# Kernel optimization log

Hardware: AMD Instinct MI355X
Metric: run time of the kernel (lower is better)

Reference implementation:

```python
import jax, jax.numpy as jnp
import numpy as np

B, V, DEMB, H, LAT, L = 16384, 64, 128, 512, 128, 2
PAD, BOS, EOS = 0, 1, 2


def setup_inputs() -> dict:
    key = jax.random.key(0)
    ks = jax.random.split(key, 12)
    s = 0.05  # small init so softmax logits stay well-scaled
    z = jax.random.normal(ks[0], (B, LAT), jnp.float32)
    E = jax.random.normal(ks[1], (V, DEMB), jnp.float32) * s
    E = E.at[PAD].set(0.0)  # padding_idx row is zero
    W_l2h = jax.random.normal(ks[2], (H, LAT), jnp.float32) * s
    b_l2h = jnp.zeros((H,), jnp.float32)
    W_ih0 = jax.random.normal(ks[3], (4 * H, DEMB), jnp.float32) * s
    W_hh0 = jax.random.normal(ks[4], (4 * H, H), jnp.float32) * s
    b_ih0 = jnp.zeros((4 * H,), jnp.float32)
    b_hh0 = jnp.zeros((4 * H,), jnp.float32)
    W_ih1 = jax.random.normal(ks[5], (4 * H, H), jnp.float32) * s
    W_hh1 = jax.random.normal(ks[6], (4 * H, H), jnp.float32) * s
    b_ih1 = jnp.zeros((4 * H,), jnp.float32)
    b_hh1 = jnp.zeros((4 * H,), jnp.float32)
    W_out = jax.random.normal(ks[7], (V, H), jnp.float32) * s
    b_out = jnp.zeros((V,), jnp.float32)
    return {"z": z, "E": E, "W_l2h": W_l2h, "b_l2h": b_l2h,
            "W_ih0": W_ih0, "W_hh0": W_hh0, "b_ih0": b_ih0, "b_hh0": b_hh0,
            "W_ih1": W_ih1, "W_hh1": W_hh1, "b_ih1": b_ih1, "b_hh1": b_hh1,
            "W_out": W_out, "b_out": b_out, "max_len": 100}


def _lstm_cell(x, h, c, Wih, Whh, bih, bhh):
    # torch LSTM gate order: i, f, g, o
    g = x @ Wih.T + bih + h @ Whh.T + bhh  # [B, 4H]
    i, f, gg, o = jnp.split(g, 4, axis=-1)
    c_new = jax.nn.sigmoid(f) * c + jax.nn.sigmoid(i) * jnp.tanh(gg)
    h_new = jax.nn.sigmoid(o) * jnp.tanh(c_new)
    return h_new, c_new


def reference(z, E, W_l2h, b_l2h, W_ih0, W_hh0, b_ih0, b_hh0,
              W_ih1, W_hh1, b_ih1, b_hh1, W_out, b_out, max_len):
    # initial states: c0 = latent2hidden(z) repeated over layers, h0 = 0
    c0 = z @ W_l2h.T + b_l2h                      # [B, H]
    c = jnp.stack([c0, c0])                       # [L, B, H]
    h = jnp.zeros_like(c)
    prev = jnp.full((B,), BOS, jnp.int32)
    is_end = jnp.zeros((B,), bool)
    keys = jax.random.split(jax.random.key(42), max_len)

    def step(carry, k):
        h, c, prev, is_end = carry
        x = E[prev]                               # [B, DEMB]
        h0, c0_ = _lstm_cell(x, h[0], c[0], W_ih0, W_hh0, b_ih0, b_hh0)
        h1, c1_ = _lstm_cell(h0, h[1], c[1], W_ih1, W_hh1, b_ih1, b_hh1)
        logits = h1 @ W_out.T + b_out             # [B, V]
        cur = jax.random.categorical(k, logits)   # same dist as Categorical(softmax(logits))
        is_end = is_end | (cur == EOS)            # mark eos; eos itself becomes pad
        cur = jnp.where(is_end, PAD, cur).astype(jnp.int32)
        return (jnp.stack([h0, h1]), jnp.stack([c0_, c1_]), cur, is_end), cur

    _, samples = jax.lax.scan(step, (h, c, prev, is_end), keys)  # [T, B]
    return samples.T                              # [B, T]
```

## Files before the change

kernel.cpp:

```cpp
#include <hip/hip_runtime.h>
#include <stdint.h>

#define B_    16384
#define V_    64
#define DEMB_ 128
#define H_    512
#define PAD_  0
#define BOS_  1
#define EOS_  2

__device__ __forceinline__ uint32_t rotl32(uint32_t v, int n) {
    return (v << n) | (v >> (32 - n));
}

__device__ __forceinline__ void tf2x32(uint32_t k0, uint32_t k1,
                                       uint32_t x0, uint32_t x1,
                                       uint32_t& o0, uint32_t& o1)
{
    const uint32_t k2 = k0 ^ k1 ^ 0x1BD11BDAu;
    x0 += k0; x1 += k1;
#define TFR(r) { x0 += x1; x1 = rotl32(x1, (r)); x1 ^= x0; }
    TFR(13) TFR(15) TFR(26) TFR(6)
    x0 += k1; x1 += k2 + 1u;
    TFR(17) TFR(29) TFR(16) TFR(24)
    x0 += k2; x1 += k0 + 2u;
    TFR(13) TFR(15) TFR(26) TFR(6)
    x0 += k0; x1 += k1 + 3u;
    TFR(17) TFR(29) TFR(16) TFR(24)
    x0 += k1; x1 += k2 + 4u;
    TFR(13) TFR(15) TFR(26) TFR(6)
    x0 += k2; x1 += k0 + 5u;
#undef TFR
    o0 = x0; o1 = x1;
}

__device__ __forceinline__ float sigm(float x) {
    return 1.0f / (1.0f + expf(-x));
}

__global__ __launch_bounds__(256)
void init_state(const float* __restrict__ z, const float* __restrict__ Wl,
                const float* __restrict__ bl,
                float* __restrict__ C0, float* __restrict__ C1,
                float* __restrict__ H0, float* __restrict__ H1)
{
    __shared__ __align__(16) float As[16][68];
    __shared__ __align__(16) float Bs[16][68];
    const int tid  = threadIdx.x;
    const int b0   = blockIdx.x * 64;
    const int j0   = blockIdx.y * 64;
    const int tx   = tid & 15, ty = tid >> 4;
    const int lrow = tid >> 2, lkq = tid & 3;

    float acc[4][4] = {};

    for (int kt = 0; kt < DEMB_ / 16; ++kt) {
        const int k0 = kt * 16;
        float4 av = *reinterpret_cast<const float4*>(z  + (size_t)(b0 + lrow) * DEMB_ + k0 + lkq * 4);
        float4 bv = *reinterpret_cast<const float4*>(Wl + (size_t)(j0 + lrow) * DEMB_ + k0 + lkq * 4);
        __syncthreads();
        As[lkq*4+0][lrow] = av.x; As[lkq*4+1][lrow] = av.y; As[lkq*4+2][lrow] = av.z; As[lkq*4+3][lrow] = av.w;
        Bs[lkq*4+0][lrow] = bv.x; Bs[lkq*4+1][lrow] = bv.y; Bs[lkq*4+2][lrow] = bv.z; Bs[lkq*4+3][lrow] = bv.w;
        __syncthreads();
#pragma unroll
        for (int kk = 0; kk < 16; ++kk) {
            float4 a4 = *reinterpret_cast<const float4*>(&As[kk][ty*4]);
            float4 b4 = *reinterpret_cast<const float4*>(&Bs[kk][tx*4]);
            float ar[4] = {a4.x, a4.y, a4.z, a4.w};
            float br[4] = {b4.x, b4.y, b4.z, b4.w};
#pragma unroll
            for (int r = 0; r < 4; ++r)
#pragma unroll
                for (int c = 0; c < 4; ++c)
                    acc[r][c] = fmaf(ar[r], br[c], acc[r][c]);
        }
    }

#pragma unroll
    for (int r = 0; r < 4; ++r) {
        const int b = b0 + ty * 4 + r;
        const int j = j0 + tx * 4;
        float v0 = acc[r][0] + bl[j+0];
        float v1 = acc[r][1] + bl[j+1];
        float v2 = acc[r][2] + bl[j+2];
        float v3 = acc[r][3] + bl[j+3];
        float4 cv = {v0, v1, v2, v3};
        float4 zz = {0.f, 0.f, 0.f, 0.f};
        *reinterpret_cast<float4*>(C0 + (size_t)b * H_ + j) = cv;
        *reinterpret_cast<float4*>(C1 + (size_t)b * H_ + j) = cv;
        *reinterpret_cast<float4*>(H0 + (size_t)b * H_ + j) = zz;
        *reinterpret_cast<float4*>(H1 + (size_t)b * H_ + j) = zz;
    }
}

__global__ __launch_bounds__(256)
void init_tokens(int* __restrict__ prevtok, int* __restrict__ isend)
{
    int i = blockIdx.x * 256 + threadIdx.x;
    if (i < B_) { prevtok[i] = BOS_; isend[i] = 0; }
}

template<int KX, bool GATHER>
__global__ __launch_bounds__(256, 2)
void lstm_layer(const float* __restrict__ Asrc,
                const int*   __restrict__ prevtok,
                const float* __restrict__ Hrec,
                const float* __restrict__ Wih,
                const float* __restrict__ Whh,
                const float* __restrict__ bih,
                const float* __restrict__ bhh,
                float* __restrict__ Cst,
                float* __restrict__ Hout)
{
    __shared__ __align__(16) float As[16][132];
    __shared__ __align__(16) float Bs[4][16][68];
    __shared__ int rowtok[128];

    const int tid  = threadIdx.x;
    const int b0   = blockIdx.x * 128;
    const int j0   = blockIdx.y * 64;
    const int tx   = tid & 15;
    const int ty   = tid >> 4;
    const int srow = tid >> 1;
    const int sk   = (tid & 1) * 8;

    if (GATHER) {
        if (tid < 128) rowtok[tid] = prevtok[b0 + tid];
        __syncthreads();
    }

    const int NT = (KX + H_) / 16;

    float4 av[2], bv[4];
    {
        const int k0 = 0;
        const float* arow = GATHER ? (Asrc + (size_t)rowtok[srow] * DEMB_)
                                   : (Asrc + (size_t)(b0 + srow) * KX);
        av[0] = *reinterpret_cast<const float4*>(arow + k0 + sk);
        av[1] = *reinterpret_cast<const float4*>(arow + k0 + sk + 4);
#pragma unroll
        for (int h = 0; h < 2; ++h) {
            const int grow = srow + h * 128;
            const int g = grow >> 6, u = grow & 63;
            const float* brow = Wih + (size_t)(g * H_ + j0 + u) * KX + k0 + sk;
            bv[h*2+0] = *reinterpret_cast<const float4*>(brow);
            bv[h*2+1] = *reinterpret_cast<const float4*>(brow + 4);
        }
    }

    float acc[4][8][4] = {};

    for (int kt = 0; kt < NT; ++kt) {
        __syncthreads();
        {
            float a0[4] = {av[0].x, av[0].y, av[0].z, av[0].w};
            float a1[4] = {av[1].x, av[1].y, av[1].z, av[1].w};
#pragma unroll
            for (int i = 0; i < 4; ++i) {
                As[sk + i][srow]     = a0[i];
                As[sk + 4 + i][srow] = a1[i];
            }
#pragma unroll
            for (int h = 0; h < 2; ++h) {
                const int grow = srow + h * 128;
                const int g = grow >> 6, u = grow & 63;
                float b0r[4] = {bv[h*2+0].x, bv[h*2+0].y, bv[h*2+0].z, bv[h*2+0].w};
                float b1r[4] = {bv[h*2+1].x, bv[h*2+1].y, bv[h*2+1].z, bv[h*2+1].w};
#pragma unroll
                for (int i = 0; i < 4; ++i) {
                    Bs[g][sk + i][u]     = b0r[i];
                    Bs[g][sk + 4 + i][u] = b1r[i];
                }
            }
        }
        __syncthreads();

        if (kt + 1 < NT) {
            const int k0n = (kt + 1) * 16;
            if (k0n < KX) {
                const float* arow = GATHER ? (Asrc + (size_t)rowtok[srow] * DEMB_)
                                           : (Asrc + (size_t)(b0 + srow) * KX);
                av[0] = *reinterpret_cast<const float4*>(arow + k0n + sk);
                av[1] = *reinterpret_cast<const float4*>(arow + k0n + sk + 4);
#pragma unroll
                for (int h = 0; h < 2; ++h) {
                    const int grow = srow + h * 128;
                    const int g = grow >> 6, u = grow & 63;
                    const float* brow = Wih + (size_t)(g * H_ + j0 + u) * KX + k0n + sk;
                    bv[h*2+0] = *reinterpret_cast<const float4*>(brow);
                    bv[h*2+1] = *reinterpret_cast<const float4*>(brow + 4);
                }
            } else {
                const int kh = k0n - KX;
                av[0] = *reinterpret_cast<const float4*>(Hrec + (size_t)(b0 + srow) * H_ + kh + sk);
                av[1] = *reinterpret_cast<const float4*>(Hrec + (size_t)(b0 + srow) * H_ + kh + sk + 4);
#pragma unroll
                for (int h = 0; h < 2; ++h) {
                    const int grow = srow + h * 128;
                    const int g = grow >> 6, u = grow & 63;
                    const float* brow = Whh + (size_t)(g * H_ + j0 + u) * H_ + kh + sk;
                    bv[h*2+0] = *reinterpret_cast<const float4*>(brow);
                    bv[h*2+1] = *reinterpret_cast<const float4*>(brow + 4);
                }
            }
        }

#pragma unroll 4
        for (int kk = 0; kk < 16; ++kk) {
            float4 a40 = *reinterpret_cast<const float4*>(&As[kk][ty*8]);
            float4 a41 = *reinterpret_cast<const float4*>(&As[kk][ty*8+4]);
            float ar[8] = {a40.x, a40.y, a40.z, a40.w, a41.x, a41.y, a41.z, a41.w};
#pragma unroll
            for (int g = 0; g < 4; ++g) {
                float4 b4 = *reinterpret_cast<const float4*>(&Bs[g][kk][tx*4]);
                float br[4] = {b4.x, b4.y, b4.z, b4.w};
#pragma unroll
                for (int r = 0; r < 8; ++r)
#pragma unroll
                    for (int c = 0; c < 4; ++c)
                        acc[g][r][c] = fmaf(ar[r], br[c], acc[g][r][c]);
            }
        }
    }

    const int j = j0 + tx * 4;
    float4 bi0 = *reinterpret_cast<const float4*>(bih + 0*H_ + j);
    float4 bi1 = *reinterpret_cast<const float4*>(bih + 1*H_ + j);
    float4 bi2 = *reinterpret_cast<const float4*>(bih + 2*H_ + j);
    float4 bi3 = *reinterpret_cast<const float4*>(bih + 3*H_ + j);
    float4 bh0 = *reinterpret_cast<const float4*>(bhh + 0*H_ + j);
    float4 bh1 = *reinterpret_cast<const float4*>(bhh + 1*H_ + j);
    float4 bh2 = *reinterpret_cast<const float4*>(bhh + 2*H_ + j);
    float4 bh3 = *reinterpret_cast<const float4*>(bhh + 3*H_ + j);
    float bi[4][4] = {{bi0.x,bi0.y,bi0.z,bi0.w},{bi1.x,bi1.y,bi1.z,bi1.w},
                      {bi2.x,bi2.y,bi2.z,bi2.w},{bi3.x,bi3.y,bi3.z,bi3.w}};
    float bh[4][4] = {{bh0.x,bh0.y,bh0.z,bh0.w},{bh1.x,bh1.y,bh1.z,bh1.w},
                      {bh2.x,bh2.y,bh2.z,bh2.w},{bh3.x,bh3.y,bh3.z,bh3.w}};

#pragma unroll
    for (int r = 0; r < 8; ++r) {
        const int b = b0 + ty * 8 + r;
        float4 c4 = *reinterpret_cast<const float4*>(Cst + (size_t)b * H_ + j);
        float cold[4] = {c4.x, c4.y, c4.z, c4.w};
        float cn[4], hn[4];
#pragma unroll
        for (int c = 0; c < 4; ++c) {
            float gi = acc[0][r][c] + bi[0][c] + bh[0][c];
            float gf = acc[1][r][c] + bi[1][c] + bh[1][c];
            float gg = acc[2][r][c] + bi[2][c] + bh[2][c];
            float go = acc[3][r][c] + bi[3][c] + bh[3][c];
            float si = sigm(gi), sf = sigm(gf), so = sigm(go);
            float tg = tanhf(gg);
            float cc = __fadd_rn(__fmul_rn(sf, cold[c]), __fmul_rn(si, tg));
            cn[c] = cc;
            hn[c] = __fmul_rn(so, tanhf(cc));
        }
        float4 co = {cn[0], cn[1], cn[2], cn[3]};
        float4 ho = {hn[0], hn[1], hn[2], hn[3]};
        *reinterpret_cast<float4*>(Cst  + (size_t)b * H_ + j) = co;
        *reinterpret_cast<float4*>(Hout + (size_t)b * H_ + j) = ho;
    }
}

__global__ __launch_bounds__(256)
void sample_step(const float* __restrict__ H1src, const float* __restrict__ Wout,
                 const float* __restrict__ bout,
                 int* __restrict__ prevtok, int* __restrict__ isend,
                 int* __restrict__ out, int t, int T)
{
    __shared__ __align__(16) float As[16][68];
    __shared__ __align__(16) float Bs[16][68];
    __shared__ float LG[64][65];

    const int tid  = threadIdx.x;
    const int b0   = blockIdx.x * 64;
    const int tx   = tid & 15, ty = tid >> 4;
    const int lrow = tid >> 2, lkq = tid & 3;

    float acc[4][4] = {};

    for (int kt = 0; kt < H_ / 16; ++kt) {
        const int k0 = kt * 16;
        float4 av = *reinterpret_cast<const float4*>(H1src + (size_t)(b0 + lrow) * H_ + k0 + lkq * 4);
        float4 bv = *reinterpret_cast<const float4*>(Wout  + (size_t)lrow * H_ + k0 + lkq * 4);
        __syncthreads();
        As[lkq*4+0][lrow] = av.x; As[lkq*4+1][lrow] = av.y; As[lkq*4+2][lrow] = av.z; As[lkq*4+3][lrow] = av.w;
        Bs[lkq*4+0][lrow] = bv.x; Bs[lkq*4+1][lrow] = bv.y; Bs[lkq*4+2][lrow] = bv.z; Bs[lkq*4+3][lrow] = bv.w;
        __syncthreads();
#pragma unroll
        for (int kk = 0; kk < 16; ++kk) {
            float4 a4 = *reinterpret_cast<const float4*>(&As[kk][ty*4]);
            float4 b4 = *reinterpret_cast<const float4*>(&Bs[kk][tx*4]);
            float ar[4] = {a4.x, a4.y, a4.z, a4.w};
            float br[4] = {b4.x, b4.y, b4.z, b4.w};
#pragma unroll
            for (int r = 0; r < 4; ++r)
#pragma unroll
                for (int c = 0; c < 4; ++c)
                    acc[r][c] = fmaf(ar[r], br[c], acc[r][c]);
        }
    }

#pragma unroll
    for (int r = 0; r < 4; ++r)
#pragma unroll
        for (int c = 0; c < 4; ++c)
            LG[ty*4 + r][tx*4 + c] = acc[r][c] + bout[tx*4 + c];
    __syncthreads();

    const int wv = tid >> 6, lane = tid & 63;
    uint32_t kt0, kt1;
    tf2x32(0u, 42u, 0u, (uint32_t)t, kt0, kt1);

    const float TINY = 1.1754943508222875e-38f;
    for (int rr = 0; rr < 16; ++rr) {
        const int r = wv * 16 + rr;
        const int b = b0 + r;
        float lg = LG[r][lane];
        uint32_t r0, r1;
        tf2x32(kt0, kt1, 0u, (uint32_t)(b * V_ + lane), r0, r1);
        uint32_t bits = r0 ^ r1;
        float f = __uint_as_float((bits >> 9) | 0x3f800000u) - 1.0f;
        float u = fmaxf(TINY, __fadd_rn(f, TINY));
        float g = -logf(-logf(u));
        float val = __fadd_rn(g, lg);
        int idx = lane;
#pragma unroll
        for (int off = 32; off > 0; off >>= 1) {
            float ov = __shfl_xor(val, off, 64);
            int   oi = __shfl_xor(idx, off, 64);
            if (ov > val || (ov == val && oi < idx)) { val = ov; idx = oi; }
        }
        if (lane == 0) {
            int cur = idx;
            int e   = isend[b];
            int en  = e | (cur == EOS_);
            int tok = en ? PAD_ : cur;
            isend[b]   = en;
            prevtok[b] = tok;
            out[(size_t)b * T + t] = tok;
        }
    }
}

extern "C" void kernel_launch(void* const* d_in, const int* in_sizes, int n_in,
                              void* d_out, int out_size, void* d_ws, size_t ws_size,
                              hipStream_t stream)
{
    (void)in_sizes; (void)n_in; (void)ws_size;
    const float* z    = (const float*)d_in[0];
    const float* E    = (const float*)d_in[1];
    const float* Wl2h = (const float*)d_in[2];
    const float* bl2h = (const float*)d_in[3];
    const float* Wih0 = (const float*)d_in[4];
    const float* Whh0 = (const float*)d_in[5];
    const float* bih0 = (const float*)d_in[6];
    const float* bhh0 = (const float*)d_in[7];
    const float* Wih1 = (const float*)d_in[8];
    const float* Whh1 = (const float*)d_in[9];
    const float* bih1 = (const float*)d_in[10];
    const float* bhh1 = (const float*)d_in[11];
    const float* Wout = (const float*)d_in[12];
    const float* bout = (const float*)d_in[13];
    int* out = (int*)d_out;
    const int T = out_size / B_;

    char* w = (char*)d_ws;
    const size_t S = (size_t)B_ * H_ * sizeof(float);
    float* C0  = (float*)(w + 0 * S);
    float* C1  = (float*)(w + 1 * S);
    float* H0A = (float*)(w + 2 * S);
    float* H0B = (float*)(w + 3 * S);
    float* H1A = (float*)(w + 4 * S);
    float* H1B = (float*)(w + 5 * S);
    int* prevtok = (int*)(w + 6 * S);
    int* isend   = (int*)(w + 6 * S + (size_t)B_ * sizeof(int));

    dim3 blk(256);
    init_state<<<dim3(B_/64, H_/64), blk, 0, stream>>>(z, Wl2h, bl2h, C0, C1, H0A, H1A);
    init_tokens<<<dim3(B_/256), blk, 0, stream>>>(prevtok, isend);

    float *h0c = H0A, *h0n = H0B, *h1c = H1A, *h1n = H1B;
    for (int t = 0; t < T; ++t) {
        lstm_layer<DEMB_, true><<<dim3(B_/128, H_/64), blk, 0, stream>>>(
            E, prevtok, h0c, Wih0, Whh0, bih0, bhh0, C0, h0n);
        lstm_layer<H_, false><<<dim3(B_/128, H_/64), blk, 0, stream>>>(
            h0n, nullptr, h1c, Wih1, Whh1, bih1, bhh1, C1, h1n);
        sample_step<<<dim3(B_/64), blk, 0, stream>>>(
            h1n, Wout, bout, prevtok, isend, out, t, T);
        float* tmp;
        tmp = h0c; h0c = h0n; h0n = tmp;
        tmp = h1c; h1c = h1n; h1n = tmp;
    }
}
```

Baseline: 134.1 ms.

## Double-buffer LDS tiles in LSTM GEMM and reorder block indexing

The LSTM layer GEMM now keeps two LDS tile buffers and prefetches two tiles ahead, so the next tile is written to shared memory while the current one is consumed, leaving one barrier per k-step instead of two. The grid becomes 1D with the 8 hidden-column blocks of the same batch rows placed on consecutive block IDs, so the activation rows they share stay hot in cache. LDS use per block roughly doubles, which could limit occupancy under the 2-blocks launch bound. The other edits only add a load helper and do not change behaviour.

Result: no change. 132.1 ms (-1.5%).

```diff
diff --git a/kernel.cpp b/kernel.cpp
--- a/kernel.cpp
+++ b/kernel.cpp
@@ -38,6 +38,10 @@
     return 1.0f / (1.0f + expf(-x));
 }
 
+__device__ __forceinline__ float4 ld4(const float* p) {
+    return *reinterpret_cast<const float4*>(p);
+}
+
 __global__ __launch_bounds__(256)
 void init_state(const float* __restrict__ z, const float* __restrict__ Wl,
                 const float* __restrict__ bl,
@@ -56,16 +60,16 @@
 
     for (int kt = 0; kt < DEMB_ / 16; ++kt) {
         const int k0 = kt * 16;
-        float4 av = *reinterpret_cast<const float4*>(z  + (size_t)(b0 + lrow) * DEMB_ + k0 + lkq * 4);
-        float4 bv = *reinterpret_cast<const float4*>(Wl + (size_t)(j0 + lrow) * DEMB_ + k0 + lkq * 4);
+        float4 av = ld4(z  + (size_t)(b0 + lrow) * DEMB_ + k0 + lkq * 4);
+        float4 bv = ld4(Wl + (size_t)(j0 + lrow) * DEMB_ + k0 + lkq * 4);
         __syncthreads();
         As[lkq*4+0][lrow] = av.x; As[lkq*4+1][lrow] = av.y; As[lkq*4+2][lrow] = av.z; As[lkq*4+3][lrow] = av.w;
         Bs[lkq*4+0][lrow] = bv.x; Bs[lkq*4+1][lrow] = bv.y; Bs[lkq*4+2][lrow] = bv.z; Bs[lkq*4+3][lrow] = bv.w;
         __syncthreads();
 #pragma unroll
         for (int kk = 0; kk < 16; ++kk) {
-            float4 a4 = *reinterpret_cast<const float4*>(&As[kk][ty*4]);
-            float4 b4 = *reinterpret_cast<const float4*>(&Bs[kk][tx*4]);
+            float4 a4 = ld4(&As[kk][ty*4]);
+            float4 b4 = ld4(&Bs[kk][tx*4]);
             float ar[4] = {a4.x, a4.y, a4.z, a4.w};
             float br[4] = {b4.x, b4.y, b4.z, b4.w};
 #pragma unroll
@@ -80,11 +84,8 @@
     for (int r = 0; r < 4; ++r) {
         const int b = b0 + ty * 4 + r;
         const int j = j0 + tx * 4;
-        float v0 = acc[r][0] + bl[j+0];
-        float v1 = acc[r][1] + bl[j+1];
-        float v2 = acc[r][2] + bl[j+2];
-        float v3 = acc[r][3] + bl[j+3];
-        float4 cv = {v0, v1, v2, v3};
+        float4 cv = {acc[r][0] + bl[j+0], acc[r][1] + bl[j+1],
+                     acc[r][2] + bl[j+2], acc[r][3] + bl[j+3]};
         float4 zz = {0.f, 0.f, 0.f, 0.f};
         *reinterpret_cast<float4*>(C0 + (size_t)b * H_ + j) = cv;
         *reinterpret_cast<float4*>(C1 + (size_t)b * H_ + j) = cv;
@@ -112,13 +113,14 @@
                 float* __restrict__ Cst,
                 float* __restrict__ Hout)
 {
-    __shared__ __align__(16) float As[16][132];
-    __shared__ __align__(16) float Bs[4][16][68];
+    __shared__ __align__(16) float As[2][16][132];
+    __shared__ __align__(16) float Bs[2][4][16][68];
     __shared__ int rowtok[128];
 
     const int tid  = threadIdx.x;
-    const int b0   = blockIdx.x * 128;
-    const int j0   = blockIdx.y * 64;
+    const int bid  = blockIdx.x;
+    const int b0   = (bid >> 3) * 128;
+    const int j0   = (bid & 7) * 64;
     const int tx   = tid & 15;
     const int ty   = tid >> 4;
     const int srow = tid >> 1;
@@ -129,90 +131,84 @@
         __syncthreads();
     }
 
+    const int grow0 = srow, grow1 = srow + 128;
+    const int g0 = grow0 >> 6, u0 = grow0 & 63;
+    const int g1 = grow1 >> 6, u1 = grow1 & 63;
+
+    const float* arowA = GATHER ? (Asrc + (size_t)rowtok[srow] * DEMB_)
+                                : (Asrc + (size_t)(b0 + srow) * KX);
+    const float* arowH = Hrec + (size_t)(b0 + srow) * H_;
+    const float* browA0 = Wih + (size_t)(g0 * H_ + j0 + u0) * KX;
+    const float* browA1 = Wih + (size_t)(g1 * H_ + j0 + u1) * KX;
+    const float* browH0 = Whh + (size_t)(g0 * H_ + j0 + u0) * H_;
+    const float* browH1 = Whh + (size_t)(g1 * H_ + j0 + u1) * H_;
+
     const int NT = (KX + H_) / 16;
 
     float4 av[2], bv[4];
-    {
-        const int k0 = 0;
-        const float* arow = GATHER ? (Asrc + (size_t)rowtok[srow] * DEMB_)
-                                   : (Asrc + (size_t)(b0 + srow) * KX);
-        av[0] = *reinterpret_cast<const float4*>(arow + k0 + sk);
-        av[1] = *reinterpret_cast<const float4*>(arow + k0 + sk + 4);
-#pragma unroll
-        for (int h = 0; h < 2; ++h) {
-            const int grow = srow + h * 128;
-            const int g = grow >> 6, u = grow & 63;
-            const float* brow = Wih + (size_t)(g * H_ + j0 + u) * KX + k0 + sk;
-            bv[h*2+0] = *reinterpret_cast<const float4*>(brow);
-            bv[h*2+1] = *reinterpret_cast<const float4*>(brow + 4);
-        }
-    }
+
+    auto load_tile = [&](int kt) {
+        const int k0 = kt * 16;
+        if (k0 < KX) {
+            av[0] = ld4(arowA + k0 + sk);
+            av[1] = ld4(arowA + k0 + sk + 4);
+            bv[0] = ld4(browA0 + k0 + sk);
+            bv[1] = ld4(browA0 + k0 + sk + 4);
+            bv[2] = ld4(browA1 + k0 + sk);
+            bv[3] = ld4(browA1 + k0 + sk + 4);
+        } else {
+            const int kh = k0 - KX;
+            av[0] = ld4(arowH + kh + sk);
+            av[1] = ld4(arowH + kh + sk + 4);
+            bv[0] = ld4(browH0 + kh + sk);
+            bv[1] = ld4(browH0 + kh + sk + 4);
+            bv[2] = ld4(browH1 + kh + sk);
+            bv[3] = ld4(browH1 + kh + sk + 4);
+        }
+    };
+
+    auto write_tile = [&](int p) {
+        float a0[4] = {av[0].x, av[0].y, av[0].z, av[0].w};
+        float a1[4] = {av[1].x, av[1].y, av[1].z, av[1].w};
+#pragma unroll
+        for (int i = 0; i < 4; ++i) {
+            As[p][sk + i][srow]     = a0[i];
+            As[p][sk + 4 + i][srow] = a1[i];
+        }
+        float b0r[4] = {bv[0].x, bv[0].y, bv[0].z, bv[0].w};
+        float b1r[4] = {bv[1].x, bv[1].y, bv[1].z, bv[1].w};
+        float b2r[4] = {bv[2].x, bv[2].y, bv[2].z, bv[2].w};
+        float b3r[4] = {bv[3].x, bv[3].y, bv[3].z, bv[3].w};
+#pragma unroll
+        for (int i = 0; i < 4; ++i) {
+            Bs[p][g0][sk + i][u0]     = b0r[i];
+            Bs[p][g0][sk + 4 + i][u0] = b1r[i];
+            Bs[p][g1][sk + i][u1]     = b2r[i];
+            Bs[p][g1][sk + 4 + i][u1] = b3r[i];
+        }
+    };
+
+    load_tile(0);
+    write_tile(0);
+    load_tile(1);
+    __syncthreads();
 
     float acc[4][8][4] = {};
 
     for (int kt = 0; kt < NT; ++kt) {
-        __syncthreads();
-        {
-            float a0[4] = {av[0].x, av[0].y, av[0].z, av[0].w};
-            float a1[4] = {av[1].x, av[1].y, av[1].z, av[1].w};
-#pragma unroll
-            for (int i = 0; i < 4; ++i) {
-                As[sk + i][srow]     = a0[i];
-                As[sk + 4 + i][srow] = a1[i];
-            }
-#pragma unroll
-            for (int h = 0; h < 2; ++h) {
-                const int grow = srow + h * 128;
-                const int g = grow >> 6, u = grow & 63;
-                float b0r[4] = {bv[h*2+0].x, bv[h*2+0].y, bv[h*2+0].z, bv[h*2+0].w};
-                float b1r[4] = {bv[h*2+1].x, bv[h*2+1].y, bv[h*2+1].z, bv[h*2+1].w};
-#pragma unroll
-                for (int i = 0; i < 4; ++i) {
-                    Bs[g][sk + i][u]     = b0r[i];
-                    Bs[g][sk + 4 + i][u] = b1r[i];
-                }
-            }
-        }
-        __syncthreads();
-
+        const int cur = kt & 1;
         if (kt + 1 < NT) {
-            const int k0n = (kt + 1) * 16;
-            if (k0n < KX) {
-                const float* arow = GATHER ? (Asrc + (size_t)rowtok[srow] * DEMB_)
-                                           : (Asrc + (size_t)(b0 + srow) * KX);
-                av[0] = *reinterpret_cast<const float4*>(arow + k0n + sk);
-                av[1] = *reinterpret_cast<const float4*>(arow + k0n + sk + 4);
-#pragma unroll
-                for (int h = 0; h < 2; ++h) {
-                    const int grow = srow + h * 128;
-                    const int g = grow >> 6, u = grow & 63;
-                    const float* brow = Wih + (size_t)(g * H_ + j0 + u) * KX + k0n + sk;
-                    bv[h*2+0] = *reinterpret_cast<const float4*>(brow);
-                    bv[h*2+1] = *reinterpret_cast<const float4*>(brow + 4);
-                }
-            } else {
-                const int kh = k0n - KX;
-                av[0] = *reinterpret_cast<const float4*>(Hrec + (size_t)(b0 + srow) * H_ + kh + sk);
-                av[1] = *reinterpret_cast<const float4*>(Hrec + (size_t)(b0 + srow) * H_ + kh + sk + 4);
-#pragma unroll
-                for (int h = 0; h < 2; ++h) {
-                    const int grow = srow + h * 128;
-                    const int g = grow >> 6, u = grow & 63;
-                    const float* brow = Whh + (size_t)(g * H_ + j0 + u) * H_ + kh + sk;
-                    bv[h*2+0] = *reinterpret_cast<const float4*>(brow);
-                    bv[h*2+1] = *reinterpret_cast<const float4*>(brow + 4);
-                }
-            }
-        }
-
+            write_tile(cur ^ 1);
+            if (kt + 2 < NT) load_tile(kt + 2);
+        }
 #pragma unroll 4
         for (int kk = 0; kk < 16; ++kk) {
-            float4 a40 = *reinterpret_cast<const float4*>(&As[kk][ty*8]);
-            float4 a41 = *reinterpret_cast<const float4*>(&As[kk][ty*8+4]);
+            float4 a40 = ld4(&As[cur][kk][ty*8]);
+            float4 a41 = ld4(&As[cur][kk][ty*8+4]);
             float ar[8] = {a40.x, a40.y, a40.z, a40.w, a41.x, a41.y, a41.z, a41.w};
 #pragma unroll
             for (int g = 0; g < 4; ++g) {
-                float4 b4 = *reinterpret_cast<const float4*>(&Bs[g][kk][tx*4]);
+                float4 b4 = ld4(&Bs[cur][g][kk][tx*4]);
                 float br[4] = {b4.x, b4.y, b4.z, b4.w};
 #pragma unroll
                 for (int r = 0; r < 8; ++r)
@@ -221,17 +217,14 @@
                         acc[g][r][c] = fmaf(ar[r], br[c], acc[g][r][c]);
             }
         }
+        __syncthreads();
     }
 
     const int j = j0 + tx * 4;
-    float4 bi0 = *reinterpret_cast<const float4*>(bih + 0*H_ + j);
-    float4 bi1 = *reinterpret_cast<const float4*>(bih + 1*H_ + j);
-    float4 bi2 = *reinterpret_cast<const float4*>(bih + 2*H_ + j);
-    float4 bi3 = *reinterpret_cast<const float4*>(bih + 3*H_ + j);
-    float4 bh0 = *reinterpret_cast<const float4*>(bhh + 0*H_ + j);
-    float4 bh1 = *reinterpret_cast<const float4*>(bhh + 1*H_ + j);
-    float4 bh2 = *reinterpret_cast<const float4*>(bhh + 2*H_ + j);
-    float4 bh3 = *reinterpret_cast<const float4*>(bhh + 3*H_ + j);
+    float4 bi0 = ld4(bih + 0*H_ + j), bi1 = ld4(bih + 1*H_ + j);
+    float4 bi2 = ld4(bih + 2*H_ + j), bi3 = ld4(bih + 3*H_ + j);
+    float4 bh0 = ld4(bhh + 0*H_ + j), bh1 = ld4(bhh + 1*H_ + j);
+    float4 bh2 = ld4(bhh + 2*H_ + j), bh3 = ld4(bhh + 3*H_ + j);
     float bi[4][4] = {{bi0.x,bi0.y,bi0.z,bi0.w},{bi1.x,bi1.y,bi1.z,bi1.w},
                       {bi2.x,bi2.y,bi2.z,bi2.w},{bi3.x,bi3.y,bi3.z,bi3.w}};
     float bh[4][4] = {{bh0.x,bh0.y,bh0.z,bh0.w},{bh1.x,bh1.y,bh1.z,bh1.w},
@@ -240,7 +233,7 @@
 #pragma unroll
     for (int r = 0; r < 8; ++r) {
         const int b = b0 + ty * 8 + r;
-        float4 c4 = *reinterpret_cast<const float4*>(Cst + (size_t)b * H_ + j);
+        float4 c4 = ld4(Cst + (size_t)b * H_ + j);
         float cold[4] = {c4.x, c4.y, c4.z, c4.w};
         float cn[4], hn[4];
 #pragma unroll
@@ -281,16 +274,16 @@
 
     for (int kt = 0; kt < H_ / 16; ++kt) {
         const int k0 = kt * 16;
-        float4 av = *reinterpret_cast<const float4*>(H1src + (size_t)(b0 + lrow) * H_ + k0 + lkq * 4);
-        float4 bv = *reinterpret_cast<const float4*>(Wout  + (size_t)lrow * H_ + k0 + lkq * 4);
+        float4 av = ld4(H1src + (size_t)(b0 + lrow) * H_ + k0 + lkq * 4);
+        float4 bv = ld4(Wout  + (size_t)lrow * H_ + k0 + lkq * 4);
         __syncthreads();
         As[lkq*4+0][lrow] = av.x; As[lkq*4+1][lrow] = av.y; As[lkq*4+2][lrow] = av.z; As[lkq*4+3][lrow] = av.w;
         Bs[lkq*4+0][lrow] = bv.x; Bs[lkq*4+1][lrow] = bv.y; Bs[lkq*4+2][lrow] = bv.z; Bs[lkq*4+3][lrow] = bv.w;
         __syncthreads();
 #pragma unroll
         for (int kk = 0; kk < 16; ++kk) {
-            float4 a4 = *reinterpret_cast<const float4*>(&As[kk][ty*4]);
-            float4 b4 = *reinterpret_cast<const float4*>(&Bs[kk][tx*4]);
+            float4 a4 = ld4(&As[kk][ty*4]);
+            float4 b4 = ld4(&Bs[kk][tx*4]);
             float ar[4] = {a4.x, a4.y, a4.z, a4.w};
             float br[4] = {b4.x, b4.y, b4.z, b4.w};
 #pragma unroll
@@ -382,9 +375,9 @@
 
     float *h0c = H0A, *h0n = H0B, *h1c = H1A, *h1n = H1B;
     for (int t = 0; t < T; ++t) {
-        lstm_layer<DEMB_, true><<<dim3(B_/128, H_/64), blk, 0, stream>>>(
+        lstm_layer<DEMB_, true><<<dim3((B_/128) * 8), blk, 0, stream>>>(
             E, prevtok, h0c, Wih0, Whh0, bih0, bhh0, C0, h0n);
-        lstm_layer<H_, false><<<dim3(B_/128, H_/64), blk, 0, stream>>>(
+        lstm_layer<H_, false><<<dim3((B_/128) * 8), blk, 0, stream>>>(
             h0n, nullptr, h1c, Wih1, Whh1, bih1, bhh1, C1, h1n);
         sample_step<<<dim3(B_/64), blk, 0, stream>>>(
             h1n, Wout, bout, prevtok, isend, out, t, T);
```
